# Kernel optimization log

Hardware: AMD Instinct MI355X
Metric: run time of the kernel (lower is better)

The kernel has to match this reference:

```python
import jax, jax.numpy as jnp
import numpy as np

NEG_SLOPE = 0.01
K = 27  # 3x3x3 kernel taps


def conv3d(x, w, b, pad):
    out = jax.lax.conv_general_dilated(
        x, w, window_strides=(1, 1, 1), padding=[(pad, pad)] * 3,
        dimension_numbers=('NCDHW', 'OIDHW', 'NCDHW'))
    return out + b[None, :, None, None, None]


def lrelu(v):
    return jnp.where(v >= 0, v, NEG_SLOPE * v)


def deform_conv3d_hw(x, offsets, w, b):
    # x: [B,C,T,H,W]; offsets: [B,2*K,T,H,W] with (dh, dw) per kernel tap;
    # depth offset is 0 ('HW' mode). Bilinear sampling in H,W, zero pad OOB.
    B, C, T, H, W = x.shape
    off = offsets.reshape(B, K, 2, T, H, W)
    dh, dw = off[:, :, 0], off[:, :, 1]  # [B,K,T,H,W]
    kidx = jnp.arange(K)
    kt = (kidx // 9)[None, :, None, None, None]
    kh = ((kidx // 3) % 3)[None, :, None, None, None]
    kw = (kidx % 3)[None, :, None, None, None]

    t_in = jnp.arange(T)[None, None, :, None, None] - 1 + kt           # int, [1,K,T,1,1]
    h_s = (jnp.arange(H)[None, None, None, :, None] - 1 + kh) + dh     # [B,K,T,H,W]
    w_s = (jnp.arange(W)[None, None, None, None, :] - 1 + kw) + dw

    t_ok = (t_in >= 0) & (t_in < T)
    t_c = jnp.clip(t_in, 0, T - 1)
    t_idx = jnp.broadcast_to(t_c, (B, K, T, H, W))
    t_ok = jnp.broadcast_to(t_ok, (B, K, T, H, W))

    h0 = jnp.floor(h_s); w0 = jnp.floor(w_s)
    fh = h_s - h0; fw = w_s - w0
    h0i = h0.astype(jnp.int32); w0i = w0.astype(jnp.int32)

    def gather_b(xb, ti, hi, wi):
        return xb[:, ti, hi, wi]  # [C,K,T,H,W]
    gather = jax.vmap(gather_b)

    cols = jnp.zeros((B, C, K, T, H, W), x.dtype)
    for ih, wgt_h in ((h0i, 1.0 - fh), (h0i + 1, fh)):
        h_ok = (ih >= 0) & (ih < H)
        ih_c = jnp.clip(ih, 0, H - 1)
        for iw, wgt_w in ((w0i, 1.0 - fw), (w0i + 1, fw)):
            w_ok = (iw >= 0) & (iw < W)
            iw_c = jnp.clip(iw, 0, W - 1)
            mask = (t_ok & h_ok & w_ok).astype(x.dtype)
            wgt = (wgt_h * wgt_w * mask)[:, None]  # [B,1,K,T,H,W]
            cols = cols + wgt * gather(x, t_idx, ih_c, iw_c)
    O = w.shape[0]
    out = jnp.einsum('bckthw,ock->bothw', cols, w.reshape(O, C, K))
    return out + b[None, :, None, None, None]


def setup_inputs() -> dict:
    key = jax.random.key(0)
    ks = jax.random.split(key, 9)
    B, Cin, Cout, T, H, W = 1, 64, 64, 8, 64, 64
    s1 = 1.0 / np.sqrt(Cin * 27)
    sr = 1.0 / np.sqrt(Cin)
    sd = 1.0 / np.sqrt(Cout * 27)
    return {
        'x': jax.random.normal(ks[0], (B, Cin, T, H, W), jnp.float32),
        'W1': jax.random.normal(ks[1], (Cout, Cin, 3, 3, 3), jnp.float32) * s1,
        'b1': jax.random.normal(ks[2], (Cout,), jnp.float32) * s1,
        'W_off': jax.random.normal(ks[3], (2 * K, Cout, 3, 3, 3), jnp.float32) * 0.01,
        'b_off': jax.random.normal(ks[4], (2 * K,), jnp.float32) * 0.01,
        'Wd': jax.random.normal(ks[5], (Cout, Cout, 3, 3, 3), jnp.float32) * sd,
        'bd': jax.random.normal(ks[6], (Cout,), jnp.float32) * sd,
        'Wr': jax.random.normal(ks[7], (Cout, Cin, 1, 1, 1), jnp.float32) * sr,
        'br': jax.random.normal(ks[8], (Cout,), jnp.float32) * sr,
    }


def reference(x, W1, b1, W_off, b_off, Wd, bd, Wr, br):
    y1 = lrelu(conv3d(x, W1, b1, pad=1))
    offsets = conv3d(y1, W_off, b_off, pad=1)          # DeformConvPack offset branch
    y2 = lrelu(deform_conv3d_hw(y1, offsets, Wd, bd))  # deformable conv, 'HW' offsets
    res = conv3d(x, Wr, br, pad=0)                     # 1x1x1 residual conv
    return y2 + res
```

## Files before the change

kernel.cpp:

```cpp
#include <hip/hip_runtime.h>
#include <hip/hip_bf16.h>

#define T_ 8
#define H_ 64
#define W_ 64
#define C_ 64
#define HW_ (H_ * W_)
#define THW_ (T_ * H_ * W_)
#define KTAPS 27
#define KDIM (C_ * KTAPS)
#define NOFF 54
#define OSTR2 58
#define AWC 35
#define AWCP 36

typedef __bf16 bf16x8 __attribute__((ext_vector_type(8)));
typedef float floatx4 __attribute__((ext_vector_type(4)));

#define LGKM_BARRIER()                                        \
    do {                                                      \
        asm volatile("s_waitcnt lgkmcnt(0)" ::: "memory");    \
        __builtin_amdgcn_s_barrier();                         \
    } while (0)

#define DECODE_SWZ_CONV(bid, t, h, wh)                        \
    const int hi3_ = (bid) & 7;                               \
    const int rest_ = (bid) >> 3;                             \
    const int wh = rest_ & 1;                                 \
    const int h = hi3_ * 8 + ((rest_ >> 1) & 7);              \
    const int t = rest_ >> 4;
#define DECODE_SWZ_ROW(bid, t, h)                             \
    const int h = ((bid) & 7) * 8 + (((bid) >> 3) & 7);       \
    const int t = (bid) >> 6;

__global__ __launch_bounds__(256) void prep_tocl_kernel(
    const float* __restrict__ x, __hip_bfloat16* __restrict__ xcl,
    const float* __restrict__ w1, const float* __restrict__ woff,
    const float* __restrict__ wd, const float* __restrict__ wr,
    __hip_bfloat16* __restrict__ w1s, __hip_bfloat16* __restrict__ woffs,
    __hip_bfloat16* __restrict__ wds, __hip_bfloat16* __restrict__ wrs) {
    __shared__ float tile[64][65];
    const int tid = threadIdx.x;

    {
        int i = blockIdx.x * 256 + tid;
        if (i < C_ * KDIM) {
            int j = i & 7, lane = (i >> 3) & 63, s = (i >> 9) & 1, g16 = (i >> 10) & 3, tap = i >> 12;
            int co = g16 * 16 + (lane & 15);
            int cin = s * 32 + (lane >> 4) * 8 + j;
            int src = (co * C_ + cin) * KTAPS + tap;
            w1s[i] = __float2bfloat16(w1[src]);
            woffs[i] = (co < NOFF) ? __float2bfloat16(woff[src]) : __float2bfloat16(0.f);
            wds[i] = __float2bfloat16(wd[src]);
        }
        if (i < C_ * C_) {
            int j = i & 7, lane = (i >> 3) & 63, s = (i >> 9) & 1, g16 = i >> 10;
            int co = g16 * 16 + (lane & 15);
            int cin = s * 32 + (lane >> 4) * 8 + j;
            wrs[i] = __float2bfloat16(wr[co * C_ + cin]);
        }
    }

    const int pos0 = blockIdx.x * 64;
    for (int i = tid; i < 4096; i += 256) {
        int ch = i >> 6, p = i & 63;
        tile[ch][p] = x[ch * THW_ + pos0 + p];
    }
    __syncthreads();
    for (int i = tid; i < 4096; i += 256) {
        int p = i >> 6, ch = i & 63;
        xcl[(pos0 + p) * C_ + ch] = __float2bfloat16(tile[ch][p]);
    }
}

__global__ __launch_bounds__(256) void conv_stream_kernel(
    const __hip_bfloat16* __restrict__ in_cl,
    const __hip_bfloat16* __restrict__ wTs,
    const float* __restrict__ bias,
    __hip_bfloat16* __restrict__ out_cl_b16) {
    __shared__ __hip_bfloat16 ts[32 * 72];
    __shared__ __hip_bfloat16 awin[3 * AWCP * C_];

    const int tid = threadIdx.x;
    const int wv = tid >> 6;
    const int lane = tid & 63;
    const int l15 = lane & 15;
    const int quad = lane >> 4;
    DECODE_SWZ_CONV(blockIdx.x, t, h, wh)
    const int w0 = wh * 32;
    const int pg = wv >> 1;
    const int chf = wv & 1;
    const int wpos = w0 + pg * 16 + l15;
    const int posbase = t * HW_ + h * W_;

    floatx4 acc0 = (floatx4){0.f, 0.f, 0.f, 0.f};
    floatx4 acc1 = (floatx4){0.f, 0.f, 0.f, 0.f};
    const bf16x8 z = {};
    const __hip_bfloat16* wb = wTs + chf * 2048 + lane * 8;

    auto rdwin = [&](int rr, int cc, int chunk) -> bf16x8 {
        const int u = (rr * AWCP + cc) * 8 + (chunk ^ (cc & 7));
        return *(const bf16x8*)((const char*)awin + u * 16);
    };

    const int ktlo = (t == 0) ? 1 : 0;
    const int kthi = (t == T_ - 1) ? 2 : 3;

#pragma unroll 1
    for (int kt = ktlo; kt < kthi; ++kt) {
        const int t_in = t - 1 + kt;

        LGKM_BARRIER();
        for (int i = tid; i < 3 * AWC * 8; i += 256) {
            const int rh = i / (AWC * 8);
            const int rem = i - rh * (AWC * 8);
            const int rw = rem >> 3;
            const int cc = rem & 7;
            const int hsrc = min(max(h - 1 + rh, 0), H_ - 1);
            const int wsrc = min(max(w0 - 1 + rw, 0), W_ - 1);
            const int u = (rh * AWCP + rw) * 8 + (cc ^ (rw & 7));
            *(bf16x8*)((char*)awin + u * 16) =
                *(const bf16x8*)&in_cl[(t_in * HW_ + hsrc * W_ + wsrc) * C_ + cc * 8];
        }
        LGKM_BARRIER();

#pragma unroll 1
        for (int kh = 0; kh < 3; ++kh) {
            const int h_in = h - 1 + kh;
            if ((unsigned)h_in >= H_) continue;
#pragma unroll
            for (int kw = 0; kw < 3; ++kw) {
                const int tap = kt * 9 + kh * 3 + kw;
                const int w_in = wpos - 1 + kw;
                const bool v = (unsigned)w_in < W_;
                const int rw = pg * 16 + l15 + kw;
                bf16x8 a0 = rdwin(kh, rw, quad);
                bf16x8 a1 = rdwin(kh, rw, quad + 4);
                a0 = v ? a0 : z;
                a1 = v ? a1 : z;
                const __hip_bfloat16* bp = wb + tap * 4096;
                const bf16x8 b00 = *(const bf16x8*)(bp);
                const bf16x8 b01 = *(const bf16x8*)(bp + 512);
                const bf16x8 b10 = *(const bf16x8*)(bp + 1024);
                const bf16x8 b11 = *(const bf16x8*)(bp + 1536);
                acc0 = __builtin_amdgcn_mfma_f32_16x16x32_bf16(a0, b00, acc0, 0, 0, 0);
                acc0 = __builtin_amdgcn_mfma_f32_16x16x32_bf16(a1, b01, acc0, 0, 0, 0);
                acc1 = __builtin_amdgcn_mfma_f32_16x16x32_bf16(a0, b10, acc1, 0, 0, 0);
                acc1 = __builtin_amdgcn_mfma_f32_16x16x32_bf16(a1, b11, acc1, 0, 0, 0);
            }
        }
    }

    const int n0 = chf * 32 + l15;
    const float bv0 = bias[n0], bv1 = bias[n0 + 16];
#pragma unroll
    for (int r = 0; r < 4; ++r) {
        const int p = pg * 16 + quad * 4 + r;
        float v0 = acc0[r] + bv0;
        v0 = (v0 >= 0.f) ? v0 : 0.01f * v0;
        float v1 = acc1[r] + bv1;
        v1 = (v1 >= 0.f) ? v1 : 0.01f * v1;
        ts[p * 72 + n0] = __float2bfloat16(v0);
        ts[p * 72 + n0 + 16] = __float2bfloat16(v1);
    }
    __syncthreads();
    {
        const int p = tid >> 3, ck = tid & 7;
        const uint4 v4 = *(const uint4*)&ts[p * 72 + ck * 8];
        *(uint4*)&out_cl_b16[(posbase + w0 + p) * C_ + ck * 8] = v4;
    }
}

struct G1 {
    bf16x8 c[4];
    float w00, w01, w10, w11;
};

__global__ __launch_bounds__(512, 4) void deform_fused_kernel(
    const __hip_bfloat16* __restrict__ y1b,
    const __hip_bfloat16* __restrict__ woffs, const float* __restrict__ boff,
    const __hip_bfloat16* __restrict__ wds, const float* __restrict__ bd,
    const __hip_bfloat16* __restrict__ xclb, const __hip_bfloat16* __restrict__ wrs,
    const float* __restrict__ br, float* __restrict__ out) {
    __shared__ __hip_bfloat16 win[6 * 64 * 64];
    __shared__ float offs[4][16][OSTR2];

    const int tid = threadIdx.x;
    const int wv = tid >> 6;
    const int lane = tid & 63;
    const int l15 = lane & 15;
    const int quad = lane >> 4;
    DECODE_SWZ_ROW(blockIdx.x, t, h)
    const int posbase = t * HW_ + h * W_;
    const int pg = wv & 3;
    const int kh2 = wv >> 2;
    const int pw = pg * 16 + l15;
    const int ch = quad + kh2 * 4;

    const int ktlo = (t == 0) ? 1 : 0;
    const int kthi = (t == T_ - 1) ? 2 : 3;

    float* winf = (float*)win;

    auto rdwin = [&](int rr, int cc, int chunk) -> bf16x8 {
        const int u = (rr * 64 + cc) * 8 + (chunk ^ (cc & 7));
        return *(const bf16x8*)((const char*)win + u * 16);
    };

    {
        floatx4 oacc[4];
#pragma unroll
        for (int g = 0; g < 4; ++g) oacc[g] = (floatx4){0.f, 0.f, 0.f, 0.f};
        const bf16x8 z = {};

#pragma unroll 1
        for (int kt = ktlo; kt < kthi; ++kt) {
            const int tin = t - 1 + kt;

            LGKM_BARRIER();
            for (int i = tid; i < 3 * 64 * 8; i += 512) {
                const int rh = i >> 9;
                const int rem = i & 511;
                const int rw = rem >> 3;
                const int cc = rem & 7;
                const int hsrc = min(max(h - 1 + rh, 0), H_ - 1);
                const int u = (rh * 64 + rw) * 8 + (cc ^ (rw & 7));
                *(bf16x8*)((char*)win + u * 16) =
                    *(const bf16x8*)&y1b[(tin * HW_ + hsrc * W_ + rw) * C_ + cc * 8];
            }
            LGKM_BARRIER();

#pragma unroll 1
            for (int kh = 0; kh < 3; ++kh) {
                const int h_in = h - 1 + kh;
                if ((unsigned)h_in >= H_) continue;
#pragma unroll
                for (int kw = 0; kw < 3; ++kw) {
                    const int tap = kt * 9 + kh * 3 + kw;
                    const int w_in = pw - 1 + kw;
                    const bool v = (unsigned)w_in < W_;
                    const int wc = v ? w_in : 0;
                    bf16x8 a = rdwin(kh, wc, ch);
                    a = v ? a : z;
                    const __hip_bfloat16* op = woffs + tap * 4096 + kh2 * 512 + lane * 8;
#pragma unroll
                    for (int g = 0; g < 4; ++g) {
                        const bf16x8 b = *(const bf16x8*)(op + g * 1024);
                        oacc[g] = __builtin_amdgcn_mfma_f32_16x16x32_bf16(a, b, oacc[g], 0, 0, 0);
                    }
                }
            }
        }
        LGKM_BARRIER();
        if (kh2 == 1) {
#pragma unroll
            for (int g = 0; g < 4; ++g)
                *(floatx4*)&winf[(pg * 64 + lane) * 16 + g * 4] = oacc[g];
        }
        LGKM_BARRIER();
        if (kh2 == 0) {
#pragma unroll
            for (int g = 0; g < 4; ++g) {
                const floatx4 p4 = *(const floatx4*)&winf[(pg * 64 + lane) * 16 + g * 4];
                oacc[g] += p4;
                const int idx = g * 16 + l15;
                if (idx < NOFF) {
                    const float bo = boff[idx];
#pragma unroll
                    for (int r = 0; r < 4; ++r)
                        offs[pg][quad * 4 + r][idx] = oacc[g][r] + bo;
                }
            }
        }
    }

    floatx4 acc[4], racc[4];
#pragma unroll
    for (int g = 0; g < 4; ++g) {
        acc[g] = (floatx4){0.f, 0.f, 0.f, 0.f};
        racc[g] = (floatx4){0.f, 0.f, 0.f, 0.f};
    }

    {
        const bf16x8 ra = *(const bf16x8*)(xclb + (posbase + pw) * C_ + ch * 8);
        const __hip_bfloat16* q = wrs + kh2 * 512 + lane * 8;
#pragma unroll
        for (int g = 0; g < 4; ++g) {
            const bf16x8 r0 = *(const bf16x8*)(q + g * 1024);
            racc[g] = __builtin_amdgcn_mfma_f32_16x16x32_bf16(ra, r0, racc[g], 0, 0, 0);
        }
    }

    auto load_off = [&](int k, float& dh, float& dw) {
        dh = offs[pg][l15][2 * k];
        dw = offs[pg][l15][2 * k + 1];
    };
    auto gatherW = [&](int k, float dh, float dw, G1& g) {
        const int kh = (k / 3) % 3, kw = k % 3;
        const float hs = (float)(h - 1 + kh) + dh;
        const float wsv = (float)(pw - 1 + kw) + dw;
        const float h0f = floorf(hs), w0f = floorf(wsv);
        const float fh = hs - h0f, fw = wsv - w0f;
        const int h0i = (int)h0f, w0i = (int)w0f;
        const int h1i = h0i + 1, w1i = w0i + 1;
        const float m_h0 = ((unsigned)h0i < H_) ? 1.f : 0.f;
        const float m_h1 = ((unsigned)h1i < H_) ? 1.f : 0.f;
        const float m_w0 = ((unsigned)w0i < W_) ? 1.f : 0.f;
        const float m_w1 = ((unsigned)w1i < W_) ? 1.f : 0.f;
        g.w00 = (1.f - fh) * (1.f - fw) * m_h0 * m_w0;
        g.w01 = (1.f - fh) * fw * m_h0 * m_w1;
        g.w10 = fh * (1.f - fw) * m_h1 * m_w0;
        g.w11 = fh * fw * m_h1 * m_w1;
        const int w0c = min(max(w0i, 0), W_ - 1);
        const int w1c = min(max(w1i, 0), W_ - 1);
        const int rh = h0i - (h - 2);
        if ((unsigned)rh <= 4u) {
            g.c[0] = rdwin(rh, w0c, ch);
            g.c[1] = rdwin(rh, w1c, ch);
            g.c[2] = rdwin(rh + 1, w0c, ch);
            g.c[3] = rdwin(rh + 1, w1c, ch);
        } else {
            const int h0c = min(max(h0i, 0), H_ - 1);
            const int h1c = min(max(h1i, 0), H_ - 1);
            const int tb = (t - 1 + k / 9) * HW_;
            g.c[0] = *(const bf16x8*)(y1b + (tb + h0c * W_ + w0c) * C_ + ch * 8);
            g.c[1] = *(const bf16x8*)(y1b + (tb + h0c * W_ + w1c) * C_ + ch * 8);
            g.c[2] = *(const bf16x8*)(y1b + (tb + h1c * W_ + w0c) * C_ + ch * 8);
            g.c[3] = *(const bf16x8*)(y1b + (tb + h1c * W_ + w1c) * C_ + ch * 8);
        }
    };
    auto blend1 = [&](const G1& g, bf16x8& fr) {
        union U { bf16x8 v; __hip_bfloat16 e[8]; };
        U c0, c1, c2, c3, r;
        c0.v = g.c[0]; c1.v = g.c[1]; c2.v = g.c[2]; c3.v = g.c[3];
#pragma unroll
        for (int j = 0; j < 8; ++j) {
            float f = g.w00 * __bfloat162float(c0.e[j]) + g.w01 * __bfloat162float(c1.e[j]) +
                      g.w10 * __bfloat162float(c2.e[j]) + g.w11 * __bfloat162float(c3.e[j]);
            r.e[j] = __float2bfloat16(f);
        }
        fr = r.v;
    };
    auto loadB = [&](int k, bf16x8& B0, bf16x8& B1, bf16x8& B2, bf16x8& B3) {
        const __hip_bfloat16* q = wds + k * 4096 + kh2 * 512 + lane * 8;
        B0 = *(const bf16x8*)(q);
        B1 = *(const bf16x8*)(q + 1024);
        B2 = *(const bf16x8*)(q + 2048);
        B3 = *(const bf16x8*)(q + 3072);
    };
    auto tapMFMA = [&](const bf16x8& fr, const bf16x8& B0, const bf16x8& B1,
                       const bf16x8& B2, const bf16x8& B3) {
        acc[0] = __builtin_amdgcn_mfma_f32_16x16x32_bf16(fr, B0, acc[0], 0, 0, 0);
        acc[1] = __builtin_amdgcn_mfma_f32_16x16x32_bf16(fr, B1, acc[1], 0, 0, 0);
        acc[2] = __builtin_amdgcn_mfma_f32_16x16x32_bf16(fr, B2, acc[2], 0, 0, 0);
        acc[3] = __builtin_amdgcn_mfma_f32_16x16x32_bf16(fr, B3, acc[3], 0, 0, 0);
    };

    G1 gA, gB;
    bf16x8 bA0, bA1, bA2, bA3, bB0, bB1, bB2, bB3;
#pragma unroll 1
    for (int kt = ktlo; kt < kthi; ++kt) {
        const int tin = t - 1 + kt;
        const int kg = kt * 9;

        LGKM_BARRIER();
        for (int i = tid; i < 6 * 64 * 8; i += 512) {
            const int rh = i >> 9;
            const int rem = i & 511;
            const int rw = rem >> 3;
            const int cc = rem & 7;
            const int hsrc = min(max(h - 2 + rh, 0), H_ - 1);
            const int u = (rh * 64 + rw) * 8 + (cc ^ (rw & 7));
            *(bf16x8*)((char*)win + u * 16) =
                *(const bf16x8*)&y1b[(tin * HW_ + hsrc * W_ + rw) * C_ + cc * 8];
        }
        LGKM_BARRIER();

        {
            float dh, dw;
            load_off(kg, dh, dw);
            gatherW(kg, dh, dw, gA);
            loadB(kg, bA0, bA1, bA2, bA3);
        }
        int k = kg;
        for (; k + 1 < kg + 9; k += 2) {
            {
                float dh, dw;
                load_off(k + 1, dh, dw);
                gatherW(k + 1, dh, dw, gB);
                loadB(k + 1, bB0, bB1, bB2, bB3);
                bf16x8 fr;
                blend1(gA, fr);
                tapMFMA(fr, bA0, bA1, bA2, bA3);
            }
            {
                if (k + 2 < kg + 9) {
                    float dh, dw;
                    load_off(k + 2, dh, dw);
                    gatherW(k + 2, dh, dw, gA);
                    loadB(k + 2, bA0, bA1, bA2, bA3);
                }
                bf16x8 fr;
                blend1(gB, fr);
                tapMFMA(fr, bB0, bB1, bB2, bB3);
            }
        }
        {
            bf16x8 fr;
            blend1(gA, fr);
            tapMFMA(fr, bA0, bA1, bA2, bA3);
        }
    }

    LGKM_BARRIER();
    if (kh2 == 1) {
#pragma unroll
        for (int g = 0; g < 4; ++g) {
            *(floatx4*)&winf[(pg * 64 + lane) * 32 + g * 4] = acc[g];
            *(floatx4*)&winf[(pg * 64 + lane) * 32 + 16 + g * 4] = racc[g];
        }
    }
    LGKM_BARRIER();
    if (kh2 == 0) {
#pragma unroll
        for (int g = 0; g < 4; ++g) {
            const floatx4 pa = *(const floatx4*)&winf[(pg * 64 + lane) * 32 + g * 4];
            const floatx4 pr = *(const floatx4*)&winf[(pg * 64 + lane) * 32 + 16 + g * 4];
            const int n = g * 16 + l15;
            const float bdv = bd[n], brv = br[n];
            floatx4 o;
#pragma unroll
            for (int r = 0; r < 4; ++r) {
                float v = acc[g][r] + pa[r] + bdv;
                v = (v >= 0.f) ? v : 0.01f * v;
                o[r] = v + racc[g][r] + pr[r] + brv;
            }
            *(floatx4*)&out[n * THW_ + posbase + pg * 16 + quad * 4] = o;
        }
    }
}

extern "C" void kernel_launch(void* const* d_in, const int* in_sizes, int n_in,
                              void* d_out, int out_size, void* d_ws, size_t ws_size,
                              hipStream_t stream) {
    const float* x    = (const float*)d_in[0];
    const float* W1   = (const float*)d_in[1];
    const float* b1   = (const float*)d_in[2];
    const float* Woff = (const float*)d_in[3];
    const float* boff = (const float*)d_in[4];
    const float* Wd   = (const float*)d_in[5];
    const float* bd   = (const float*)d_in[6];
    const float* Wr   = (const float*)d_in[7];
    const float* br   = (const float*)d_in[8];
    float* out = (float*)d_out;

    float* ws = (float*)d_ws;
    __hip_bfloat16* xclb  = (__hip_bfloat16*)(ws);
    __hip_bfloat16* y1b   = (__hip_bfloat16*)(ws + 1048576);
    __hip_bfloat16* w1s   = (__hip_bfloat16*)(ws + 2097152);
    __hip_bfloat16* woffs = (__hip_bfloat16*)(ws + 2152448);
    __hip_bfloat16* wdsb  = (__hip_bfloat16*)(ws + 2207744);
    __hip_bfloat16* wrsb  = (__hip_bfloat16*)(ws + 2263040);

    prep_tocl_kernel<<<THW_ / 64, 256, 0, stream>>>(
        x, xclb, W1, Woff, Wd, Wr, w1s, woffs, wdsb, wrsb);

    conv_stream_kernel<<<dim3(T_ * H_ * 2), 256, 0, stream>>>(
        xclb, w1s, b1, y1b);

    deform_fused_kernel<<<dim3(T_ * H_), 512, 0, stream>>>(
        y1b, woffs, boff, wdsb, bd, xclb, wrsb, br, out);
}
```

Before: 146.2 us.

## Software-pipeline conv tap loads and shrink deform LDS window to five rows

The conv kernel's tap loop is flattened and double-buffered: the weight and LDS window operands for the next tap are fetched while the MFMAs for the current tap run. The first tap's weights are issued before the barrier. Out-of-range H rows are now masked to zero instead of skipped, so those taps still execute their MFMAs. Separately, the deform kernel's LDS window drops from six to five rows, which lowers LDS use and may raise occupancy, but more samples fall back to global memory gathers.

```diff
diff --git a/kernel.cpp b/kernel.cpp
--- a/kernel.cpp
+++ b/kernel.cpp
@@ -11,8 +11,6 @@
 #define KDIM (C_ * KTAPS)
 #define NOFF 54
 #define OSTR2 58
-#define AWC 35
-#define AWCP 36
 
 typedef __bf16 bf16x8 __attribute__((ext_vector_type(8)));
 typedef float floatx4 __attribute__((ext_vector_type(4)));
@@ -79,7 +77,7 @@
     const float* __restrict__ bias,
     __hip_bfloat16* __restrict__ out_cl_b16) {
     __shared__ __hip_bfloat16 ts[32 * 72];
-    __shared__ __hip_bfloat16 awin[3 * AWCP * C_];
+    __shared__ __hip_bfloat16 awin[3 * 36 * C_];
 
     const int tid = threadIdx.x;
     const int wv = tid >> 6;
@@ -99,8 +97,33 @@
     const __hip_bfloat16* wb = wTs + chf * 2048 + lane * 8;
 
     auto rdwin = [&](int rr, int cc, int chunk) -> bf16x8 {
-        const int u = (rr * AWCP + cc) * 8 + (chunk ^ (cc & 7));
+        const int u = (rr * 36 + cc) * 8 + (chunk ^ (cc & 7));
         return *(const bf16x8*)((const char*)awin + u * 16);
+    };
+    auto fetch = [&](int kt, int k, bf16x8& a0, bf16x8& a1,
+                     bf16x8& B0, bf16x8& B1, bf16x8& B2, bf16x8& B3) {
+        const int kh = k / 3, kw = k % 3;
+        const __hip_bfloat16* bp = wb + (kt * 9 + k) * 4096;
+        B0 = *(const bf16x8*)(bp);
+        B1 = *(const bf16x8*)(bp + 512);
+        B2 = *(const bf16x8*)(bp + 1024);
+        B3 = *(const bf16x8*)(bp + 1536);
+        const int rw = pg * 16 + l15 + kw;
+        a0 = rdwin(kh, rw, quad);
+        a1 = rdwin(kh, rw, quad + 4);
+    };
+    auto compute = [&](int k, bf16x8 a0, bf16x8 a1, const bf16x8& B0,
+                       const bf16x8& B1, const bf16x8& B2, const bf16x8& B3) {
+        const int kh = k / 3, kw = k % 3;
+        const int h_in = h - 1 + kh;
+        const int w_in = wpos - 1 + kw;
+        const bool v = ((unsigned)h_in < H_) && ((unsigned)w_in < W_);
+        a0 = v ? a0 : z;
+        a1 = v ? a1 : z;
+        acc0 = __builtin_amdgcn_mfma_f32_16x16x32_bf16(a0, B0, acc0, 0, 0, 0);
+        acc0 = __builtin_amdgcn_mfma_f32_16x16x32_bf16(a1, B1, acc0, 0, 0, 0);
+        acc1 = __builtin_amdgcn_mfma_f32_16x16x32_bf16(a0, B2, acc1, 0, 0, 0);
+        acc1 = __builtin_amdgcn_mfma_f32_16x16x32_bf16(a1, B3, acc1, 0, 0, 0);
     };
 
     const int ktlo = (t == 0) ? 1 : 0;
@@ -111,44 +134,41 @@
         const int t_in = t - 1 + kt;
 
         LGKM_BARRIER();
-        for (int i = tid; i < 3 * AWC * 8; i += 256) {
-            const int rh = i / (AWC * 8);
-            const int rem = i - rh * (AWC * 8);
+        for (int i = tid; i < 3 * 35 * 8; i += 256) {
+            const int rh = i / (35 * 8);
+            const int rem = i - rh * (35 * 8);
             const int rw = rem >> 3;
             const int cc = rem & 7;
             const int hsrc = min(max(h - 1 + rh, 0), H_ - 1);
             const int wsrc = min(max(w0 - 1 + rw, 0), W_ - 1);
-            const int u = (rh * AWCP + rw) * 8 + (cc ^ (rw & 7));
+            const int u = (rh * 36 + rw) * 8 + (cc ^ (rw & 7));
             *(bf16x8*)((char*)awin + u * 16) =
                 *(const bf16x8*)&in_cl[(t_in * HW_ + hsrc * W_ + wsrc) * C_ + cc * 8];
         }
-        LGKM_BARRIER();
-
-#pragma unroll 1
-        for (int kh = 0; kh < 3; ++kh) {
-            const int h_in = h - 1 + kh;
-            if ((unsigned)h_in >= H_) continue;
-#pragma unroll
-            for (int kw = 0; kw < 3; ++kw) {
-                const int tap = kt * 9 + kh * 3 + kw;
-                const int w_in = wpos - 1 + kw;
-                const bool v = (unsigned)w_in < W_;
-                const int rw = pg * 16 + l15 + kw;
-                bf16x8 a0 = rdwin(kh, rw, quad);
-                bf16x8 a1 = rdwin(kh, rw, quad + 4);
-                a0 = v ? a0 : z;
-                a1 = v ? a1 : z;
-                const __hip_bfloat16* bp = wb + tap * 4096;
-                const bf16x8 b00 = *(const bf16x8*)(bp);
-                const bf16x8 b01 = *(const bf16x8*)(bp + 512);
-                const bf16x8 b10 = *(const bf16x8*)(bp + 1024);
-                const bf16x8 b11 = *(const bf16x8*)(bp + 1536);
-                acc0 = __builtin_amdgcn_mfma_f32_16x16x32_bf16(a0, b00, acc0, 0, 0, 0);
-                acc0 = __builtin_amdgcn_mfma_f32_16x16x32_bf16(a1, b01, acc0, 0, 0, 0);
-                acc1 = __builtin_amdgcn_mfma_f32_16x16x32_bf16(a0, b10, acc1, 0, 0, 0);
-                acc1 = __builtin_amdgcn_mfma_f32_16x16x32_bf16(a1, b11, acc1, 0, 0, 0);
-            }
-        }
+        bf16x8 sAa0, sAa1, sAb0, sAb1, sAb2, sAb3;
+        bf16x8 sBa0, sBa1, sBb0, sBb1, sBb2, sBb3;
+        {
+            const __hip_bfloat16* bp = wb + (kt * 9) * 4096;
+            sAb0 = *(const bf16x8*)(bp);
+            sAb1 = *(const bf16x8*)(bp + 512);
+            sAb2 = *(const bf16x8*)(bp + 1024);
+            sAb3 = *(const bf16x8*)(bp + 1536);
+        }
+        LGKM_BARRIER();
+        {
+            const int rw = pg * 16 + l15;
+            sAa0 = rdwin(0, rw, quad);
+            sAa1 = rdwin(0, rw, quad + 4);
+        }
+
+        int k = 0;
+        for (; k + 1 < 9; k += 2) {
+            fetch(kt, k + 1, sBa0, sBa1, sBb0, sBb1, sBb2, sBb3);
+            compute(k, sAa0, sAa1, sAb0, sAb1, sAb2, sAb3);
+            if (k + 2 < 9) fetch(kt, k + 2, sAa0, sAa1, sAb0, sAb1, sAb2, sAb3);
+            compute(k + 1, sBa0, sBa1, sBb0, sBb1, sBb2, sBb3);
+        }
+        compute(8, sAa0, sAa1, sAb0, sAb1, sAb2, sAb3);
     }
 
     const int n0 = chf * 32 + l15;
@@ -182,7 +202,7 @@
     const __hip_bfloat16* __restrict__ wds, const float* __restrict__ bd,
     const __hip_bfloat16* __restrict__ xclb, const __hip_bfloat16* __restrict__ wrs,
     const float* __restrict__ br, float* __restrict__ out) {
-    __shared__ __hip_bfloat16 win[6 * 64 * 64];
+    __shared__ __hip_bfloat16 win[5 * 64 * 64];
     __shared__ float offs[4][16][OSTR2];
 
     const int tid = threadIdx.x;
@@ -314,7 +334,7 @@
         const int w0c = min(max(w0i, 0), W_ - 1);
         const int w1c = min(max(w1i, 0), W_ - 1);
         const int rh = h0i - (h - 2);
-        if ((unsigned)rh <= 4u) {
+        if ((unsigned)rh <= 3u) {
             g.c[0] = rdwin(rh, w0c, ch);
             g.c[1] = rdwin(rh, w1c, ch);
             g.c[2] = rdwin(rh + 1, w0c, ch);
@@ -364,7 +384,7 @@
         const int kg = kt * 9;
 
         LGKM_BARRIER();
-        for (int i = tid; i < 6 * 64 * 8; i += 512) {
+        for (int i = tid; i < 5 * 64 * 8; i += 512) {
             const int rh = i >> 9;
             const int rem = i & 511;
             const int rw = rem >> 3;
```

Measured after the change: 145.3 us. Within noise of the previous version (-0.6%).
